# Kernel optimization log

Measured on AMD Instinct MI355X. Metric: run time of the kernel, lower is better.

The kernel has to match this reference:

```python
import math
import jax, jax.numpy as jnp
import numpy as np

B, S, DK, DV = 8, 2048, 512, 512

def setup_inputs() -> dict:
    key = jax.random.key(0)
    kq, kk, kv, km = jax.random.split(key, 4)
    Q = jax.random.normal(kq, (B, S, DK), dtype=jnp.float32)
    K = jax.random.normal(kk, (B, S, DK), dtype=jnp.float32)
    V = jax.random.normal(kv, (B, S, DV), dtype=jnp.float32)
    # key-padding mask, True = masked out; broadcasts over query dim
    mask_out = jax.random.randint(km, (B, 1, S), 0, 2).astype(jnp.bool_)
    return {"Q": Q, "K": K, "V": V, "mask_out": mask_out}

def reference(Q, K, V, mask_out):
    scale = math.sqrt(Q.shape[-1])
    # [B, S, S] scores
    scores = jnp.einsum('bqd,bkd->bqk', Q, K) / scale
    scores = jnp.where(mask_out, -jnp.inf, scores)
    attn = jax.nn.softmax(scores, axis=-1)
    # dropout is identity in eval mode (reference baseline)
    return jnp.einsum('bqk,bkv->bqv', attn, V)
```

## Files before the change

kernel.cpp:

```cpp
#include <hip/hip_runtime.h>
#include <stdint.h>
#include <stddef.h>

#define B_ 8
#define S_ 2048
#define D_ 512
#define QT 32
#define KTL 32
#define NIT (S_ / KTL)

typedef __attribute__((ext_vector_type(8))) short short8;
typedef __attribute__((ext_vector_type(4))) float f32x4;

#define OFF_K   0
#define OFF_V   32768
#define OFF_ST  65536
#define OFF_P   69632
#define OFF_A   71680
#define OFF_L   71808
#define OFF_M   71936
#define LDS_BYTES 72192

__device__ __forceinline__ void gl_lds16(const void* g, void* l) {
  __builtin_amdgcn_global_load_lds(
      (const __attribute__((address_space(1))) uint32_t*)g,
      (__attribute__((address_space(3))) uint32_t*)l, 16, 0, 0);
}

__device__ __forceinline__ uint32_t f2bf(float f) {
  union { float f; uint32_t u; } x; x.f = f;
  uint32_t r = x.u + 0x7FFFu + ((x.u >> 16) & 1u);
  return r >> 16;
}

__device__ __forceinline__ bool sniff_fp32(const void* p) {
  const uint32_t* w = (const uint32_t*)p;
  bool ok = true;
  #pragma unroll 1
  for (int i = 0; i < 64; ++i) {
    uint32_t e = (w[i] >> 23) & 0xFFu;
    if (!(e == 0u || (e >= 64u && e <= 192u))) ok = false;
  }
  return ok;
}

__device__ __forceinline__ short8 cvt8(const void* src, bool fp32) {
  short8 d;
  if (fp32) {
    const float* s = (const float*)src;
    f32x4 a = *(const f32x4*)s, c = *(const f32x4*)(s + 4);
    #pragma unroll
    for (int j = 0; j < 4; ++j) { d[j] = (short)f2bf(a[j]); d[4 + j] = (short)f2bf(c[j]); }
  } else {
    d = *(const short8*)src;
  }
  return d;
}

__global__ void kbf_kernel(const void* __restrict__ in, uint16_t* __restrict__ out) {
  bool fp32 = sniff_fp32(in);
  size_t i = ((size_t)blockIdx.x * 256 + threadIdx.x) * 8;
  const void* src = fp32 ? (const void*)((const float*)in + i)
                         : (const void*)((const uint16_t*)in + i);
  *(short8*)(out + i) = cvt8(src, fp32);
}

__global__ void vt_kernel(const void* __restrict__ V, uint16_t* __restrict__ vt) {
  bool fp32 = sniff_fp32(V);
  int kt = blockIdx.x, dt = blockIdx.y, b = blockIdx.z;
  int t  = threadIdx.x;
  int dv = t >> 3;
  int kg = t & 7;
  int dvg = dt * 64 + dv;
  size_t base = (size_t)b * S_ * D_;
  short8 o;
  #pragma unroll
  for (int j = 0; j < 8; ++j) {
    size_t off = base + (size_t)(kt * 64 + kg * 8 + j) * D_ + dvg;
    if (fp32) o[j] = (short)f2bf(((const float*)V)[off]);
    else      o[j] = (short)((const uint16_t*)V)[off];
  }
  *(short8*)(vt + ((size_t)b * D_ + dvg) * S_ + kt * 64 + kg * 8) = o;
}

__device__ __forceinline__ void stage_K(char* smem, const uint16_t* kg, int w, int lane, int kt) {
  #pragma unroll
  for (int p = 0; p < 8; ++p) {
    int n = p * 4 + w;
    int g = (lane & ~7) | ((lane ^ n) & 7);
    gl_lds16(kg + ((size_t)(kt * KTL + n)) * D_ + g * 8, smem + OFF_K + (p * 4 + w) * 1024);
  }
}
__device__ __forceinline__ void stage_VT(char* smem, const uint16_t* vtg, int w, int lane, int kt) {
  #pragma unroll
  for (int p = 0; p < 8; ++p) {
    int dvl = p * 16 + (lane >> 2);
    int g = (lane & 3) ^ (dvl & 3);
    gl_lds16(vtg + ((size_t)(w * 128 + dvl)) * S_ + kt * KTL + g * 8,
             smem + OFF_V + w * 8192 + p * 1024);
  }
}
__device__ __forceinline__ void stage_K_slow(char* smem, const void* kg, bool fp32,
                                             int w, int lane, int kt) {
  #pragma unroll
  for (int p = 0; p < 8; ++p) {
    int n = p * 4 + w;
    size_t off = ((size_t)(kt * KTL + n)) * D_ + lane * 8;
    const void* src = fp32 ? (const void*)((const float*)kg + off)
                           : (const void*)((const uint16_t*)kg + off);
    short8 d = cvt8(src, fp32);
    int s = (lane & ~7) | ((lane ^ n) & 7);
    *(short8*)(smem + OFF_K + n * 1024 + s * 16) = d;
  }
}
__device__ __forceinline__ void stage_V_slow(char* smem, const void* vg, bool fp32,
                                             int w, int lane, int kt) {
  #pragma unroll
  for (int p = 0; p < 8; ++p) {
    int n = p * 4 + w;
    size_t off = ((size_t)(kt * KTL + n)) * D_ + lane * 8;
    const void* src = fp32 ? (const void*)((const float*)vg + off)
                           : (const void*)((const uint16_t*)vg + off);
    short8 d = cvt8(src, fp32);
    *(short8*)(smem + OFF_V + n * 1024 + lane * 16) = d;
  }
}

template<bool FAST>
__global__ __launch_bounds__(256, 2)
void attn_kernel(const void* __restrict__ Q, const void* __restrict__ K,
                 const void* __restrict__ V, const void* __restrict__ mask,
                 const uint16_t* __restrict__ kbf, const uint16_t* __restrict__ vtbf,
                 void* __restrict__ out) {
  extern __shared__ char smem[];
  const int tid  = threadIdx.x;
  const int lane = tid & 63;
  const int w    = tid >> 6;
  const int m15  = lane & 15;
  const int kq   = lane >> 4;

  const bool fp32 = sniff_fp32(Q);

  const int b     = blockIdx.x;
  const int qbase = blockIdx.y * QT;
  const int rt_qk = w >> 1;
  const int cb_qk = (w & 1) * 16;

  const uint16_t* kgf  = FAST ? (kbf + (size_t)b * S_ * D_) : nullptr;
  const uint16_t* vtgf = FAST ? (vtbf + (size_t)b * D_ * S_) : nullptr;
  const void* kgs = fp32 ? (const void*)((const float*)K + (size_t)b * S_ * D_)
                         : (const void*)((const uint16_t*)K + (size_t)b * S_ * D_);
  const void* vgs = fp32 ? (const void*)((const float*)V + (size_t)b * S_ * D_)
                         : (const void*)((const uint16_t*)V + (size_t)b * S_ * D_);

  if (tid < 64) {
    const uint32_t* mw = (const uint32_t*)mask;
    const uint8_t*  mb = (const uint8_t*)mask;
    bool is64 = true, any_even = false, is32 = true;
    for (int j = 0; j < 64; ++j) {
      uint32_t lo = mw[2 * j], hi = mw[2 * j + 1];
      if (hi != 0u || lo > 1u) is64 = false;
      if (lo) any_even = true;
    }
    is64 = is64 && any_even;
    for (int j = 0; j < 128; ++j) {
      uint32_t x = mw[j];
      if (x != 0u && x != 1u && x != 0x3F800000u) is32 = false;
    }
    uint32_t bits = 0;
    int base = b * S_ + tid * 32;
    for (int e = 0; e < 32; ++e) {
      uint32_t x = is64 ? mw[2 * (base + e)]
                        : (is32 ? mw[base + e] : (uint32_t)mb[base + e]);
      bits |= (x ? 1u : 0u) << e;
    }
    *(uint32_t*)(smem + OFF_M + tid * 4) = bits;
  }

  short8 aq[16];
  {
    size_t q0 = ((size_t)b * S_ + qbase + rt_qk * 16 + m15) * D_ + kq * 8;
    #pragma unroll
    for (int sl = 0; sl < 16; ++sl) {
      size_t off = q0 + sl * 32;
      const void* src = fp32 ? (const void*)((const float*)Q + off)
                             : (const void*)((const uint16_t*)Q + off);
      aq[sl] = cvt8(src, fp32);
    }
  }

  f32x4 acc_o[2][8];
  #pragma unroll
  for (int i = 0; i < 2; ++i)
    #pragma unroll
    for (int j = 0; j < 8; ++j)
      acc_o[i][j] = (f32x4){0.f, 0.f, 0.f, 0.f};

  float m_run = -1e30f, l_run = 0.f;
  const float k1 = 0.06375872f;

  if (FAST) { stage_K(smem, kgf, w, lane, 0); stage_VT(smem, vtgf, w, lane, 0); }

  for (int kt = 0; kt < NIT; ++kt) {
    if (!FAST) {
      __syncthreads();
      stage_K_slow(smem, kgs, fp32, w, lane, kt);
      stage_V_slow(smem, vgs, fp32, w, lane, kt);
    }
    __syncthreads();

    int keyg = kt * KTL + cb_qk + m15;
    float bv = ((*(const uint32_t*)(smem + OFF_M + (keyg >> 5) * 4) >> (keyg & 31)) & 1u)
               ? -3.0e38f : 0.f;

    f32x4 acc_s = (f32x4){0.f, 0.f, 0.f, 0.f};
    #pragma unroll
    for (int sl = 0; sl < 16; ++sl) {
      int n  = cb_qk + m15;
      int c  = sl * 4 + kq;
      int cs = (c & ~7) | ((c ^ n) & 7);
      short8 bf = *(const short8*)(smem + OFF_K + n * 1024 + cs * 16);
      acc_s = __builtin_amdgcn_mfma_f32_16x16x32_bf16(aq[sl], bf, acc_s, 0, 0, 0);
    }

    {
      int key  = cb_qk + m15;
      int blk  = rt_qk * 4 + kq;
      int xblk = blk ^ (key & 7);
      f32x4 sv;
      #pragma unroll
      for (int r = 0; r < 4; ++r) sv[r] = acc_s[r] * k1 + bv;
      *(f32x4*)(smem + OFF_ST + key * 128 + xblk * 16) = sv;
    }
    __syncthreads();

    if (FAST && kt < NIT - 1) stage_K(smem, kgf, w, lane, kt + 1);

    {
      int r  = w * 8 + (lane >> 3);
      int k0 = (lane & 7) * 4;
      float u[4];
      #pragma unroll
      for (int i = 0; i < 4; ++i) {
        int k    = k0 + i;
        int xblk = (r >> 2) ^ (k & 7);
        u[i] = *(const float*)(smem + OFF_ST + k * 128 + xblk * 16 + (r & 3) * 4);
      }
      float mt = fmaxf(fmaxf(u[0], u[1]), fmaxf(u[2], u[3]));
      mt = fmaxf(mt, __shfl_xor(mt, 1, 64));
      mt = fmaxf(mt, __shfl_xor(mt, 2, 64));
      mt = fmaxf(mt, __shfl_xor(mt, 4, 64));
      float m_new = fmaxf(m_run, mt);
      float alpha = exp2f(m_run - m_new);
      float s = 0.f;
      #pragma unroll
      for (int i = 0; i < 4; ++i) { u[i] = exp2f(u[i] - m_new); s += u[i]; }
      s += __shfl_xor(s, 1, 64);
      s += __shfl_xor(s, 2, 64);
      s += __shfl_xor(s, 4, 64);
      l_run = l_run * alpha + s;
      m_run = m_new;
      uint2 d;
      d.x = f2bf(u[0]) | (f2bf(u[1]) << 16);
      d.y = f2bf(u[2]) | (f2bf(u[3]) << 16);
      *(uint2*)(smem + OFF_P + r * 64 + k0 * 2) = d;
      if ((lane & 7) == 0) {
        *(float*)(smem + OFF_A + r * 4) = alpha;
        *(float*)(smem + OFF_L + r * 4) = l_run;
      }
    }
    __syncthreads();

    #pragma unroll
    for (int rt = 0; rt < 2; ++rt) {
      f32x4 al = *(const f32x4*)(smem + OFF_A + (rt * 16 + kq * 4) * 4);
      #pragma unroll
      for (int ct = 0; ct < 8; ++ct) acc_o[rt][ct] *= al;
    }
    short8 ap[2];
    #pragma unroll
    for (int rt = 0; rt < 2; ++rt)
      ap[rt] = *(const short8*)(smem + OFF_P + (rt * 16 + m15) * 64 + kq * 16);
    #pragma unroll
    for (int ct = 0; ct < 8; ++ct) {
      short8 bvv;
      if (FAST) {
        int dvL = ct * 16 + m15;
        int cs  = kq ^ (dvL & 3);
        bvv = *(const short8*)(smem + OFF_V + w * 8192 + dvL * 64 + cs * 16);
      } else {
        #pragma unroll
        for (int j = 0; j < 8; ++j)
          bvv[j] = *(const short*)(smem + OFF_V + (kq * 8 + j) * 1024
                                   + (w * 128 + ct * 16 + m15) * 2);
      }
      #pragma unroll
      for (int rt = 0; rt < 2; ++rt)
        acc_o[rt][ct] = __builtin_amdgcn_mfma_f32_16x16x32_bf16(
            ap[rt], bvv, acc_o[rt][ct], 0, 0, 0);
    }

    if (FAST && kt < NIT - 1) stage_VT(smem, vtgf, w, lane, kt + 1);
  }

  #pragma unroll
  for (int rt = 0; rt < 2; ++rt) {
    f32x4 lv = *(const f32x4*)(smem + OFF_L + (rt * 16 + kq * 4) * 4);
    f32x4 inv;
    #pragma unroll
    for (int r = 0; r < 4; ++r) inv[r] = lv[r] > 0.f ? 1.f / lv[r] : 0.f;
    #pragma unroll
    for (int ct = 0; ct < 8; ++ct) {
      int col = w * 128 + ct * 16 + m15;
      #pragma unroll
      for (int r = 0; r < 4; ++r) {
        int row = qbase + rt * 16 + kq * 4 + r;
        size_t idx = ((size_t)b * S_ + row) * D_ + col;
        float val = acc_o[rt][ct][r] * inv[r];
        if (fp32) ((float*)out)[idx] = val;
        else      ((uint16_t*)out)[idx] = (uint16_t)f2bf(val);
      }
    }
  }
}

extern "C" void kernel_launch(void* const* d_in, const int* in_sizes, int n_in,
                              void* d_out, int out_size, void* d_ws, size_t ws_size,
                              hipStream_t stream) {
  (void)in_sizes; (void)n_in; (void)out_size;
  const void* Q    = d_in[0];
  const void* K    = d_in[1];
  const void* V    = d_in[2];
  const void* mask = d_in[3];

  const size_t half = (size_t)B_ * S_ * D_ * 2;
  bool fast = ws_size >= 2 * half;

  if (fast) {
    uint16_t* kbf  = (uint16_t*)d_ws;
    uint16_t* vtbf = (uint16_t*)((char*)d_ws + half);
    kbf_kernel<<<4096, 256, 0, stream>>>(K, kbf);
    vt_kernel<<<dim3(32, 8, 8), 512, 0, stream>>>(V, vtbf);
    hipFuncSetAttribute((const void*)attn_kernel<true>,
                        hipFuncAttributeMaxDynamicSharedMemorySize, LDS_BYTES);
    attn_kernel<true><<<dim3(8, S_ / QT), 256, LDS_BYTES, stream>>>(
        Q, K, V, mask, kbf, vtbf, d_out);
  } else {
    hipFuncSetAttribute((const void*)attn_kernel<false>,
                        hipFuncAttributeMaxDynamicSharedMemorySize, LDS_BYTES);
    attn_kernel<false><<<dim3(8, S_ / QT), 256, LDS_BYTES, stream>>>(
        Q, K, V, mask, nullptr, nullptr, d_out);
  }
}
```

Before: 338.5 us.

## Double Q tile to 64 rows with 512 threads, double-buffer K, load V from global

Raises the query tile to 64 rows per block with 8 waves, which halves the number of times each K/V tile is streamed per query. K tiles are double-buffered in LDS using async global-to-LDS loads with custom waitcnt barriers, while V^T fragments are read straight from global memory into registers instead of being staged through LDS. The two prep kernels are merged into one launch. This trades more LDS and higher per-block register pressure for better reuse and fewer barriers, at the risk of lower occupancy and V load latency ending up on the critical path.

```diff
diff --git a/kernel.cpp b/kernel.cpp
--- a/kernel.cpp
+++ b/kernel.cpp
@@ -5,26 +5,39 @@
 #define B_ 8
 #define S_ 2048
 #define D_ 512
-#define QT 32
+#define QT 64
 #define KTL 32
 #define NIT (S_ / KTL)
 
 typedef __attribute__((ext_vector_type(8))) short short8;
 typedef __attribute__((ext_vector_type(4))) float f32x4;
 
-#define OFF_K   0
-#define OFF_V   32768
+#define OFF_K0  0
+#define OFF_K1  32768
 #define OFF_ST  65536
-#define OFF_P   69632
-#define OFF_A   71680
-#define OFF_L   71808
-#define OFF_M   71936
-#define LDS_BYTES 72192
+#define OFF_P   73728
+#define OFF_A   77824
+#define OFF_L   78080
+#define OFF_M   78336
+#define LDS_BYTES 78592
 
 __device__ __forceinline__ void gl_lds16(const void* g, void* l) {
   __builtin_amdgcn_global_load_lds(
       (const __attribute__((address_space(1))) uint32_t*)g,
       (__attribute__((address_space(3))) uint32_t*)l, 16, 0, 0);
+}
+
+__device__ __forceinline__ void bar_lgkm() {
+  __asm__ __volatile__("" ::: "memory");
+  __builtin_amdgcn_s_waitcnt(0xC07F);
+  __builtin_amdgcn_s_barrier();
+  __asm__ __volatile__("" ::: "memory");
+}
+__device__ __forceinline__ void bar_vm0() {
+  __asm__ __volatile__("" ::: "memory");
+  __builtin_amdgcn_s_waitcnt(0x0070);
+  __builtin_amdgcn_s_barrier();
+  __asm__ __volatile__("" ::: "memory");
 }
 
 __device__ __forceinline__ uint32_t f2bf(float f) {
@@ -57,77 +70,68 @@
   return d;
 }
 
-__global__ void kbf_kernel(const void* __restrict__ in, uint16_t* __restrict__ out) {
-  bool fp32 = sniff_fp32(in);
-  size_t i = ((size_t)blockIdx.x * 256 + threadIdx.x) * 8;
-  const void* src = fp32 ? (const void*)((const float*)in + i)
-                         : (const void*)((const uint16_t*)in + i);
-  *(short8*)(out + i) = cvt8(src, fp32);
-}
-
-__global__ void vt_kernel(const void* __restrict__ V, uint16_t* __restrict__ vt) {
-  bool fp32 = sniff_fp32(V);
+__global__ void prep_kernel(const void* __restrict__ K, const void* __restrict__ V,
+                            uint16_t* __restrict__ kbf, uint16_t* __restrict__ vt) {
+  bool fp32 = sniff_fp32(K);
   int kt = blockIdx.x, dt = blockIdx.y, b = blockIdx.z;
   int t  = threadIdx.x;
-  int dv = t >> 3;
-  int kg = t & 7;
-  int dvg = dt * 64 + dv;
-  size_t base = (size_t)b * S_ * D_;
-  short8 o;
-  #pragma unroll
-  for (int j = 0; j < 8; ++j) {
-    size_t off = base + (size_t)(kt * 64 + kg * 8 + j) * D_ + dvg;
-    if (fp32) o[j] = (short)f2bf(((const float*)V)[off]);
-    else      o[j] = (short)((const uint16_t*)V)[off];
-  }
-  *(short8*)(vt + ((size_t)b * D_ + dvg) * S_ + kt * 64 + kg * 8) = o;
-}
-
-__device__ __forceinline__ void stage_K(char* smem, const uint16_t* kg, int w, int lane, int kt) {
-  #pragma unroll
-  for (int p = 0; p < 8; ++p) {
-    int n = p * 4 + w;
+  {
+    size_t off = (size_t)b * S_ * D_ + (size_t)(kt * 64 + (t >> 3)) * D_ + dt * 64 + (t & 7) * 8;
+    const void* src = fp32 ? (const void*)((const float*)K + off)
+                           : (const void*)((const uint16_t*)K + off);
+    *(short8*)(kbf + off) = cvt8(src, fp32);
+  }
+  {
+    int dvg = dt * 64 + (t >> 3);
+    int kg  = t & 7;
+    size_t base = (size_t)b * S_ * D_;
+    short8 o;
+    #pragma unroll
+    for (int j = 0; j < 8; ++j) {
+      size_t off = base + (size_t)(kt * 64 + kg * 8 + j) * D_ + dvg;
+      if (fp32) o[j] = (short)f2bf(((const float*)V)[off]);
+      else      o[j] = (short)((const uint16_t*)V)[off];
+    }
+    *(short8*)(vt + ((size_t)b * D_ + dvg) * S_ + kt * 64 + kg * 8) = o;
+  }
+}
+
+__device__ __forceinline__ void stage_K(char* buf, const uint16_t* kg, int w, int lane, int kt) {
+  #pragma unroll
+  for (int p = 0; p < 4; ++p) {
+    int n = p * 8 + w;
     int g = (lane & ~7) | ((lane ^ n) & 7);
-    gl_lds16(kg + ((size_t)(kt * KTL + n)) * D_ + g * 8, smem + OFF_K + (p * 4 + w) * 1024);
-  }
-}
-__device__ __forceinline__ void stage_VT(char* smem, const uint16_t* vtg, int w, int lane, int kt) {
-  #pragma unroll
-  for (int p = 0; p < 8; ++p) {
-    int dvl = p * 16 + (lane >> 2);
-    int g = (lane & 3) ^ (dvl & 3);
-    gl_lds16(vtg + ((size_t)(w * 128 + dvl)) * S_ + kt * KTL + g * 8,
-             smem + OFF_V + w * 8192 + p * 1024);
-  }
-}
-__device__ __forceinline__ void stage_K_slow(char* smem, const void* kg, bool fp32,
+    gl_lds16(kg + ((size_t)(kt * KTL + n)) * D_ + g * 8, buf + n * 1024);
+  }
+}
+__device__ __forceinline__ void stage_K_slow(char* buf, const void* kg, bool fp32,
                                              int w, int lane, int kt) {
   #pragma unroll
-  for (int p = 0; p < 8; ++p) {
-    int n = p * 4 + w;
+  for (int p = 0; p < 4; ++p) {
+    int n = p * 8 + w;
     size_t off = ((size_t)(kt * KTL + n)) * D_ + lane * 8;
     const void* src = fp32 ? (const void*)((const float*)kg + off)
                            : (const void*)((const uint16_t*)kg + off);
     short8 d = cvt8(src, fp32);
     int s = (lane & ~7) | ((lane ^ n) & 7);
-    *(short8*)(smem + OFF_K + n * 1024 + s * 16) = d;
+    *(short8*)(buf + n * 1024 + s * 16) = d;
   }
 }
 __device__ __forceinline__ void stage_V_slow(char* smem, const void* vg, bool fp32,
                                              int w, int lane, int kt) {
   #pragma unroll
-  for (int p = 0; p < 8; ++p) {
-    int n = p * 4 + w;
+  for (int p = 0; p < 4; ++p) {
+    int n = p * 8 + w;
     size_t off = ((size_t)(kt * KTL + n)) * D_ + lane * 8;
     const void* src = fp32 ? (const void*)((const float*)vg + off)
                            : (const void*)((const uint16_t*)vg + off);
     short8 d = cvt8(src, fp32);
-    *(short8*)(smem + OFF_V + n * 1024 + lane * 16) = d;
+    *(short8*)(smem + OFF_K1 + n * 1024 + lane * 16) = d;
   }
 }
 
 template<bool FAST>
-__global__ __launch_bounds__(256, 2)
+__global__ __launch_bounds__(512, 2)
 void attn_kernel(const void* __restrict__ Q, const void* __restrict__ K,
                  const void* __restrict__ V, const void* __restrict__ mask,
                  const uint16_t* __restrict__ kbf, const uint16_t* __restrict__ vtbf,
@@ -143,11 +147,11 @@
 
   const int b     = blockIdx.x;
   const int qbase = blockIdx.y * QT;
-  const int rt_qk = w >> 1;
-  const int cb_qk = (w & 1) * 16;
+  const int qt_w  = w >> 1;
+  const int kh    = w & 1;
 
   const uint16_t* kgf  = FAST ? (kbf + (size_t)b * S_ * D_) : nullptr;
-  const uint16_t* vtgf = FAST ? (vtbf + (size_t)b * D_ * S_) : nullptr;
+  const uint16_t* vtg  = FAST ? (vtbf + (size_t)b * D_ * S_) : nullptr;
   const void* kgs = fp32 ? (const void*)((const float*)K + (size_t)b * S_ * D_)
                          : (const void*)((const uint16_t*)K + (size_t)b * S_ * D_);
   const void* vgs = fp32 ? (const void*)((const float*)V + (size_t)b * S_ * D_)
@@ -179,7 +183,7 @@
 
   short8 aq[16];
   {
-    size_t q0 = ((size_t)b * S_ + qbase + rt_qk * 16 + m15) * D_ + kq * 8;
+    size_t q0 = ((size_t)b * S_ + qbase + qt_w * 16 + m15) * D_ + kq * 8;
     #pragma unroll
     for (int sl = 0; sl < 16; ++sl) {
       size_t off = q0 + sl * 32;
@@ -189,52 +193,63 @@
     }
   }
 
-  f32x4 acc_o[2][8];
-  #pragma unroll
-  for (int i = 0; i < 2; ++i)
-    #pragma unroll
-    for (int j = 0; j < 8; ++j)
+  f32x4 acc_o[4][4];
+  #pragma unroll
+  for (int i = 0; i < 4; ++i)
+    #pragma unroll
+    for (int j = 0; j < 4; ++j)
       acc_o[i][j] = (f32x4){0.f, 0.f, 0.f, 0.f};
 
   float m_run = -1e30f, l_run = 0.f;
   const float k1 = 0.06375872f;
 
-  if (FAST) { stage_K(smem, kgf, w, lane, 0); stage_VT(smem, vtgf, w, lane, 0); }
+  if (FAST) stage_K(smem + OFF_K0, kgf, w, lane, 0);
 
   for (int kt = 0; kt < NIT; ++kt) {
-    if (!FAST) {
+    char* kbuf = smem + ((kt & 1) && FAST ? OFF_K1 : OFF_K0);
+    if (FAST) {
+      bar_vm0();
+    } else {
       __syncthreads();
-      stage_K_slow(smem, kgs, fp32, w, lane, kt);
+      stage_K_slow(smem + OFF_K0, kgs, fp32, w, lane, kt);
       stage_V_slow(smem, vgs, fp32, w, lane, kt);
-    }
-    __syncthreads();
-
-    int keyg = kt * KTL + cb_qk + m15;
+      __syncthreads();
+    }
+
+    short8 vf[4];
+    if (FAST) {
+      #pragma unroll
+      for (int ct = 0; ct < 4; ++ct)
+        vf[ct] = *(const short8*)(vtg + (size_t)(w * 64 + ct * 16 + m15) * S_
+                                  + kt * KTL + kq * 8);
+      if (kt < NIT - 1)
+        stage_K(smem + ((kt & 1) ? OFF_K0 : OFF_K1), kgf, w, lane, kt + 1);
+    }
+
+    int keyg = kt * KTL + kh * 16 + m15;
     float bv = ((*(const uint32_t*)(smem + OFF_M + (keyg >> 5) * 4) >> (keyg & 31)) & 1u)
                ? -3.0e38f : 0.f;
 
     f32x4 acc_s = (f32x4){0.f, 0.f, 0.f, 0.f};
     #pragma unroll
     for (int sl = 0; sl < 16; ++sl) {
-      int n  = cb_qk + m15;
+      int n  = kh * 16 + m15;
       int c  = sl * 4 + kq;
       int cs = (c & ~7) | ((c ^ n) & 7);
-      short8 bf = *(const short8*)(smem + OFF_K + n * 1024 + cs * 16);
+      short8 bf = *(const short8*)(kbuf + n * 1024 + cs * 16);
       acc_s = __builtin_amdgcn_mfma_f32_16x16x32_bf16(aq[sl], bf, acc_s, 0, 0, 0);
     }
 
     {
-      int key  = cb_qk + m15;
-      int blk  = rt_qk * 4 + kq;
-      int xblk = blk ^ (key & 7);
+      int key  = kh * 16 + m15;
+      int blk  = qt_w * 4 + kq;
+      int xblk = blk ^ (key & 15) ^ ((key >> 2) & 3);
       f32x4 sv;
       #pragma unroll
       for (int r = 0; r < 4; ++r) sv[r] = acc_s[r] * k1 + bv;
-      *(f32x4*)(smem + OFF_ST + key * 128 + xblk * 16) = sv;
-    }
-    __syncthreads();
-
-    if (FAST && kt < NIT - 1) stage_K(smem, kgf, w, lane, kt + 1);
+      *(f32x4*)(smem + OFF_ST + key * 256 + xblk * 16) = sv;
+    }
+    bar_lgkm();
 
     {
       int r  = w * 8 + (lane >> 3);
@@ -243,8 +258,8 @@
       #pragma unroll
       for (int i = 0; i < 4; ++i) {
         int k    = k0 + i;
-        int xblk = (r >> 2) ^ (k & 7);
-        u[i] = *(const float*)(smem + OFF_ST + k * 128 + xblk * 16 + (r & 3) * 4);
+        int xblk = (r >> 2) ^ (k & 15) ^ ((k >> 2) & 3);
+        u[i] = *(const float*)(smem + OFF_ST + k * 256 + xblk * 16 + (r & 3) * 4);
       }
       float mt = fmaxf(fmaxf(u[0], u[1]), fmaxf(u[2], u[3]));
       mt = fmaxf(mt, __shfl_xor(mt, 1, 64));
@@ -269,49 +284,45 @@
         *(float*)(smem + OFF_L + r * 4) = l_run;
       }
     }
-    __syncthreads();
-
-    #pragma unroll
-    for (int rt = 0; rt < 2; ++rt) {
+    bar_lgkm();
+
+    #pragma unroll
+    for (int rt = 0; rt < 4; ++rt) {
       f32x4 al = *(const f32x4*)(smem + OFF_A + (rt * 16 + kq * 4) * 4);
       #pragma unroll
-      for (int ct = 0; ct < 8; ++ct) acc_o[rt][ct] *= al;
-    }
-    short8 ap[2];
-    #pragma unroll
-    for (int rt = 0; rt < 2; ++rt)
+      for (int ct = 0; ct < 4; ++ct) acc_o[rt][ct] *= al;
+    }
+    short8 ap[4];
+    #pragma unroll
+    for (int rt = 0; rt < 4; ++rt)
       ap[rt] = *(const short8*)(smem + OFF_P + (rt * 16 + m15) * 64 + kq * 16);
     #pragma unroll
-    for (int ct = 0; ct < 8; ++ct) {
+    for (int ct = 0; ct < 4; ++ct) {
       short8 bvv;
       if (FAST) {
-        int dvL = ct * 16 + m15;
-        int cs  = kq ^ (dvL & 3);
-        bvv = *(const short8*)(smem + OFF_V + w * 8192 + dvL * 64 + cs * 16);
+        bvv = vf[ct];
       } else {
         #pragma unroll
         for (int j = 0; j < 8; ++j)
-          bvv[j] = *(const short*)(smem + OFF_V + (kq * 8 + j) * 1024
-                                   + (w * 128 + ct * 16 + m15) * 2);
+          bvv[j] = *(const short*)(smem + OFF_K1 + (kq * 8 + j) * 1024
+                                   + (w * 64 + ct * 16 + m15) * 2);
       }
       #pragma unroll
-      for (int rt = 0; rt < 2; ++rt)
+      for (int rt = 0; rt < 4; ++rt)
         acc_o[rt][ct] = __builtin_amdgcn_mfma_f32_16x16x32_bf16(
             ap[rt], bvv, acc_o[rt][ct], 0, 0, 0);
     }
-
-    if (FAST && kt < NIT - 1) stage_VT(smem, vtgf, w, lane, kt + 1);
-  }
-
-  #pragma unroll
-  for (int rt = 0; rt < 2; ++rt) {
+  }
+
+  #pragma unroll
+  for (int rt = 0; rt < 4; ++rt) {
     f32x4 lv = *(const f32x4*)(smem + OFF_L + (rt * 16 + kq * 4) * 4);
     f32x4 inv;
     #pragma unroll
     for (int r = 0; r < 4; ++r) inv[r] = lv[r] > 0.f ? 1.f / lv[r] : 0.f;
     #pragma unroll
-    for (int ct = 0; ct < 8; ++ct) {
-      int col = w * 128 + ct * 16 + m15;
+    for (int ct = 0; ct < 4; ++ct) {
+      int col = w * 64 + ct * 16 + m15;
       #pragma unroll
       for (int r = 0; r < 4; ++r) {
         int row = qbase + rt * 16 + kq * 4 + r;
@@ -339,16 +350,15 @@
   if (fast) {
     uint16_t* kbf  = (uint16_t*)d_ws;
     uint16_t* vtbf = (uint16_t*)((char*)d_ws + half);
-    kbf_kernel<<<4096, 256, 0, stream>>>(K, kbf);
-    vt_kernel<<<dim3(32, 8, 8), 512, 0, stream>>>(V, vtbf);
+    prep_kernel<<<dim3(32, 8, 8), 512, 0, stream>>>(K, V, kbf, vtbf);
     hipFuncSetAttribute((const void*)attn_kernel<true>,
                         hipFuncAttributeMaxDynamicSharedMemorySize, LDS_BYTES);
-    attn_kernel<true><<<dim3(8, S_ / QT), 256, LDS_BYTES, stream>>>(
+    attn_kernel<true><<<dim3(8, S_ / QT), 512, LDS_BYTES, stream>>>(
         Q, K, V, mask, kbf, vtbf, d_out);
   } else {
     hipFuncSetAttribute((const void*)attn_kernel<false>,
                         hipFuncAttributeMaxDynamicSharedMemorySize, LDS_BYTES);
-    attn_kernel<false><<<dim3(8, S_ / QT), 256, LDS_BYTES, stream>>>(
+    attn_kernel<false><<<dim3(8, S_ / QT), 512, LDS_BYTES, stream>>>(
         Q, K, V, mask, nullptr, nullptr, d_out);
   }
 }
```

Result: faster. 298.8 us (-11.7%).
